# Optimization experiments

Measured on AMD Instinct MI355X. Metric: run time of the kernel, lower is better.

## Reference

```python
import jax, jax.numpy as jnp
import numpy as np

EPS = 1e-8

def div_small(a, b):
    b_safe = b * (b > EPS) + (b <= EPS) * EPS
    return a / b_safe

def cos_full(q1h, q2h, w):
    # q1h [b,s1,h], q2h [b,s1_or_1,h], w [P,h] -> [b,s1,P]
    a = q1h[:, :, None, :] * w          # [b,s1,P,h]
    c = q2h[:, :, None, :] * w          # [b,s1|1,P,h]
    num = jnp.sum(a * c, axis=-1)
    den = jnp.maximum(jnp.linalg.norm(a, axis=-1) * jnp.linalg.norm(c, axis=-1), EPS)
    return num / den

def cos_maxpool(q1h, q2h, w):
    # q1h [b,s1,h], q2h [b,s2,h], w [P,h] -> max over s2 of cosine -> [b,s1,P]
    a = q1h[:, :, None, :] * w          # [b,s1,P,h]
    c = q2h[:, :, None, :] * w          # [b,s2,P,h]
    num = jnp.einsum('biph,bjph->bijp', a, c)            # [b,s1,s2,P]
    na = jnp.linalg.norm(a, axis=-1)                     # [b,s1,P]
    nc = jnp.linalg.norm(c, axis=-1)                     # [b,s2,P]
    den = jnp.maximum(na[:, :, None, :] * nc[:, None, :, :], EPS)
    return jnp.max(num / den, axis=2)

def attention(q1, q2):
    # cosine-similarity matrix [b,s1,s2]
    n1 = jnp.linalg.norm(q1, axis=2, keepdims=True)      # [b,s1,1]
    n2 = jnp.linalg.norm(q2, axis=2, keepdims=True)      # [b,s2,1]
    num = jnp.einsum('bih,bjh->bij', q1, q2)
    return div_small(num, n1 * jnp.swapaxes(n2, 1, 2))

def setup_inputs() -> dict:
    key = jax.random.key(0)
    k1, k2, kw = jax.random.split(key, 3)
    q1_batch = jax.random.normal(k1, (16, 128, 512), dtype=jnp.float32)
    q2_batch = jax.random.normal(k2, (16, 128, 512), dtype=jnp.float32)
    W = jax.random.normal(kw, (8, 16, 256), dtype=jnp.float32)
    return {"q1_batch": q1_batch, "q2_batch": q2_batch, "W": W}

def reference(q1_batch, q2_batch, W):
    h = q1_batch.shape[-1] // 2
    q1_fw, q1_bw = q1_batch[..., :h], q1_batch[..., h:]
    q2_fw, q2_bw = q2_batch[..., :h], q2_batch[..., h:]

    # 1) full matching against last (fw) / first (bw) q2 state
    full_fw = cos_full(q1_fw, q2_fw[:, -1:, :], W[0])
    full_bw = cos_full(q1_bw, q2_bw[:, :1, :], W[1])

    # 2) max-pool matching over all q2 positions
    max_fw = cos_maxpool(q1_fw, q2_fw, W[2])
    max_bw = cos_maxpool(q1_bw, q2_bw, W[3])

    # 3) attentive matching
    att_fw = attention(q1_fw, q2_fw)                     # [b,s1,s2]
    att_bw = attention(q1_bw, q2_bw)
    at_q2_fw = att_fw[..., None] * q2_fw[:, None, :, :]  # [b,s1,s2,h]
    at_q2_bw = att_bw[..., None] * q2_bw[:, None, :, :]
    mean_fw = div_small(at_q2_fw.sum(axis=2), att_fw.sum(axis=2, keepdims=True))
    # NOTE: denominator intentionally uses att_fw (bug preserved from source)
    mean_bw = div_small(at_q2_bw.sum(axis=2), att_fw.sum(axis=2, keepdims=True))
    attn_fw = cos_full(q1_fw, mean_fw, W[4])
    attn_bw = cos_full(q1_bw, mean_bw, W[5])

    # 4) max-attentive matching
    max_at_fw = at_q2_fw.max(axis=2)                     # [b,s1,h]
    max_at_bw = at_q2_bw.max(axis=2)
    maxattn_fw = cos_full(q1_fw, max_at_fw, W[6])
    maxattn_bw = cos_full(q1_bw, max_at_bw, W[7])

    return jnp.concatenate(
        [full_fw, full_bw, max_fw, max_bw, attn_fw, attn_bw, maxattn_fw, maxattn_bw],
        axis=-1)
```

## Files before the change

kernel.cpp:

```cpp
#include <hip/hip_runtime.h>
#include <hip/hip_bf16.h>

#define B 16
#define L 128
#define H 256
#define H2 512
#define P 16
#define EPSF 1e-8f
#define LDSTR 72

typedef __attribute__((ext_vector_type(8))) short short8;
typedef __attribute__((ext_vector_type(4))) short short4v;
typedef __attribute__((ext_vector_type(4))) float f32x4;

__device__ __forceinline__ short f2bf(float x) {
    unsigned u = __builtin_bit_cast(unsigned, x);
    u += 0x7fffu + ((u >> 16) & 1u);
    return (short)(u >> 16);
}
__device__ __forceinline__ float bf2f(short s) {
    unsigned u = ((unsigned)(unsigned short)s) << 16;
    return __builtin_bit_cast(float, u);
}
__device__ __forceinline__ short8 pack8(float4 x, float4 y) {
    short8 s;
    s[0] = f2bf(x.x); s[1] = f2bf(x.y); s[2] = f2bf(x.z); s[3] = f2bf(x.w);
    s[4] = f2bf(y.x); s[5] = f2bf(y.y); s[6] = f2bf(y.z); s[7] = f2bf(y.w);
    return s;
}
__device__ __forceinline__ float dot4(float4 v) {
    return v.x * v.x + v.y * v.y + v.z * v.z + v.w * v.w;
}
__device__ __forceinline__ float4 mul4(float4 a, float4 b) {
    return make_float4(a.x * b.x, a.y * b.y, a.z * b.z, a.w * b.w);
}

__global__ void __launch_bounds__(64) k_att_v3(
        const float* __restrict__ q1, const float* __restrict__ q2,
        float* __restrict__ att_fw, float* __restrict__ att_bw,
        float* __restrict__ attsum) {
    int bx = blockIdx.x;
    int b = bx >> 1, dir = bx & 1;
    int m0 = blockIdx.y * 16, n0 = blockIdx.z * 16;
    int l = threadIdx.x, q = l >> 4, coll = l & 15;
    size_t bL = (size_t)b * L;

    const float* arow = q1 + (bL + m0 + coll) * H2 + dir * H;
    const float* brow = q2 + (bL + n0 + coll) * H2 + dir * H;

    f32x4 acc = (f32x4){0.f, 0.f, 0.f, 0.f};
    float na = 0.f, nc = 0.f;
#pragma unroll
    for (int ks = 0; ks < 8; ks++) {
        int koff = ks * 32 + q * 8;
        float4 a0 = *(const float4*)(arow + koff);
        float4 a1 = *(const float4*)(arow + koff + 4);
        float4 b0 = *(const float4*)(brow + koff);
        float4 b1 = *(const float4*)(brow + koff + 4);
        na += dot4(a0) + dot4(a1);
        nc += dot4(b0) + dot4(b1);
        short8 af = pack8(a0, a1);
        short8 bf = pack8(b0, b1);
        acc = __builtin_amdgcn_mfma_f32_16x16x32_bf16(af, bf, acc, 0, 0, 0);
    }
    na += __shfl_xor(na, 16); na += __shfl_xor(na, 32);
    nc += __shfl_xor(nc, 16); nc += __shfl_xor(nc, 32);
    float na_s = sqrtf(na), nc_s = sqrtf(nc);

    float* attout = dir ? att_bw : att_fw;
    float rsum[4];
#pragma unroll
    for (int r = 0; r < 4; r++) {
        float nar = __shfl(na_s, (l & 48) + q * 4 + r);
        float den = nar * nc_s;
        den = den > EPSF ? den : EPSF;
        float a = acc[r] / den;
        attout[(bL + m0 + q * 4 + r) * L + n0 + coll] = a;
        rsum[r] = a;
    }
    if (dir == 0) {
#pragma unroll
        for (int off = 1; off < 16; off <<= 1)
#pragma unroll
            for (int r = 0; r < 4; r++)
                rsum[r] += __shfl_xor(rsum[r], off, 16);
        if (coll == 0)
#pragma unroll
            for (int r = 0; r < 4; r++)
                atomicAdd(&attsum[bL + m0 + q * 4 + r], rsum[r]);
    }
}

__global__ void __launch_bounds__(256) k_meanmax_v3(
        const float* __restrict__ q2,
        const float* __restrict__ att_fw, const float* __restrict__ att_bw,
        const float* __restrict__ attsum,
        float* __restrict__ mean_fw, float* __restrict__ mean_bw,
        float* __restrict__ maxat_fw, float* __restrict__ maxat_bw) {
    int bd = blockIdx.x;
    int b = bd >> 1, dir = bd & 1;
    int i0 = blockIdx.y * 4;
    int t = threadIdx.x;
    int wave = t >> 6, l = t & 63;
    size_t bL = (size_t)b * L;

    __shared__ float at[4][L];
    __shared__ float Ss[4];
    __shared__ f32x4 red[4][64][4];

    const float* att = dir ? att_bw : att_fw;
    for (int v = t; v < 4 * L; v += 256)
        at[v >> 7][v & 127] = att[(bL + i0 + (v >> 7)) * L + (v & 127)];
    if (t < 4) {
        float s = attsum[bL + i0 + t];
        Ss[t] = s > EPSF ? s : EPSF;
    }
    __syncthreads();

    f32x4 sum[4], mx[4];
#pragma unroll
    for (int r = 0; r < 4; r++) {
        sum[r] = (f32x4){0.f, 0.f, 0.f, 0.f};
        mx[r] = (f32x4){-INFINITY, -INFINITY, -INFINITY, -INFINITY};
    }
    const float* q2b = q2 + bL * H2 + dir * H;
    for (int jj = 0; jj < 32; jj++) {
        int j = wave * 32 + jj;
        float4 c = *(const float4*)(q2b + (size_t)j * H2 + l * 4);
#pragma unroll
        for (int r = 0; r < 4; r++) {
            float w = at[r][j];
            f32x4 v = { w * c.x, w * c.y, w * c.z, w * c.w };
            sum[r] += v;
            mx[r][0] = fmaxf(mx[r][0], v[0]);
            mx[r][1] = fmaxf(mx[r][1], v[1]);
            mx[r][2] = fmaxf(mx[r][2], v[2]);
            mx[r][3] = fmaxf(mx[r][3], v[3]);
        }
    }
    float* meanout = dir ? mean_bw : mean_fw;
    float* maxout = dir ? maxat_bw : maxat_fw;
    for (int rr = 0; rr < 2; rr++) {
        __syncthreads();
        red[wave][l][0] = sum[rr * 2];
        red[wave][l][1] = mx[rr * 2];
        red[wave][l][2] = sum[rr * 2 + 1];
        red[wave][l][3] = mx[rr * 2 + 1];
        __syncthreads();
        if (t < 128) {
            int r2 = t >> 6;
            int lane = t & 63;
            f32x4 s = red[0][lane][r2 * 2];
            f32x4 m = red[0][lane][r2 * 2 + 1];
            for (int w = 1; w < 4; w++) {
                s += red[w][lane][r2 * 2];
                f32x4 m2 = red[w][lane][r2 * 2 + 1];
                m[0] = fmaxf(m[0], m2[0]);
                m[1] = fmaxf(m[1], m2[1]);
                m[2] = fmaxf(m[2], m2[2]);
                m[3] = fmaxf(m[3], m2[3]);
            }
            int row = i0 + rr * 2 + r2;
            float inv = 1.f / Ss[rr * 2 + r2];
            size_t o = (bL + row) * H + lane * 4;
            *(f32x4*)(meanout + o) = s * inv;
            *(f32x4*)(maxout + o) = m;
        }
    }
}

__global__ void __launch_bounds__(256) k_cosfull_v3(
        const float* __restrict__ q1, const float* __restrict__ q2,
        const float* __restrict__ mean_fw, const float* __restrict__ mean_bw,
        const float* __restrict__ maxat_fw, const float* __restrict__ maxat_bw,
        const float* __restrict__ W, float* __restrict__ out) {
    int bg = blockIdx.x;
    int b = bg >> 4;
    int i0 = (bg & 15) * 8;
    int piece = blockIdx.y;
    int t = threadIdx.x;
    int p = t >> 4, l = t & 15;
    size_t bL = (size_t)b * L;

    int widx, colb, dir, cstride;
    const float* cptr;
    switch (piece) {
        case 0: widx = 0; colb = 0;   dir = 0; cptr = q2 + (bL + L - 1) * H2;  cstride = 0; break;
        case 1: widx = 1; colb = 16;  dir = 1; cptr = q2 + bL * H2 + H;        cstride = 0; break;
        case 2: widx = 4; colb = 64;  dir = 0; cptr = mean_fw + bL * H;        cstride = H; break;
        case 3: widx = 5; colb = 80;  dir = 1; cptr = mean_bw + bL * H;        cstride = H; break;
        case 4: widx = 6; colb = 96;  dir = 0; cptr = maxat_fw + bL * H;       cstride = H; break;
        default: widx = 7; colb = 112; dir = 1; cptr = maxat_bw + bL * H;      cstride = H; break;
    }
    const float* wrow = W + ((size_t)widx * P + p) * H;
    float wsq[16];
#pragma unroll
    for (int k = 0; k < 16; k++) {
        float wv = wrow[l + 16 * k];
        wsq[k] = wv * wv;
    }
    for (int ii = 0; ii < 8; ii++) {
        int i = i0 + ii;
        const float* r1 = q1 + (bL + i) * H2 + dir * H;
        const float* crow = cptr + (size_t)i * cstride;
        float num = 0, na = 0, nc = 0;
#pragma unroll
        for (int k = 0; k < 16; k++) {
            int h = l + 16 * k;
            float a = r1[h];
            float c = crow[h];
            num += a * c * wsq[k];
            na  += a * a * wsq[k];
            nc  += c * c * wsq[k];
        }
        for (int off = 8; off; off >>= 1) {
            num += __shfl_down(num, off, 16);
            na  += __shfl_down(na,  off, 16);
            nc  += __shfl_down(nc,  off, 16);
        }
        if (l == 0) {
            float den = sqrtf(na) * sqrtf(nc);
            den = den > EPSF ? den : EPSF;
            out[(bL + i) * 128 + colb + p] = num / den;
        }
    }
}

__global__ void __launch_bounds__(256) k_maxpool_v2(
        const float* __restrict__ q1, const float* __restrict__ q2,
        const float* __restrict__ W, float* __restrict__ out) {
    int bd = blockIdx.x;
    int b = bd >> 1, dir = bd & 1;
    int p = blockIdx.y;
    int t = threadIdx.x;
    int wave = t >> 6, l = t & 63;
    int q = l >> 4, coll = l & 15;
    int m0 = blockIdx.z * 64 + wave * 16;
    size_t bL = (size_t)b * L;

    __shared__ short Bs[128 * LDSTR];
    __shared__ float wf[H];
    __shared__ float ncs[128];

    if (t < 64)
        *(float4*)(wf + t * 4) =
            *(const float4*)(W + ((size_t)(2 + dir) * P + p) * H + t * 4);
    __syncthreads();

    f32x4 acc[8];
#pragma unroll
    for (int nt = 0; nt < 8; nt++) acc[nt] = (f32x4){0.f, 0.f, 0.f, 0.f};
    float ncp = 0.f, nap = 0.f;

    int brow = t >> 1, bc0 = (t & 1) * 32;
    const float* q1b = q1 + bL * H2 + dir * H;
    const float* q2b = q2 + bL * H2 + dir * H;
    const float* arow = q1b + (size_t)(m0 + coll) * H2;
    const float* brp = q2b + (size_t)brow * H2;

    for (int kt = 0; kt < 4; kt++) {
        int k0 = kt * 64;
#pragma unroll
        for (int cc = 0; cc < 8; cc++) {
            float4 v = *(const float4*)(brp + k0 + bc0 + cc * 4);
            float4 wv4 = *(const float4*)(wf + k0 + bc0 + cc * 4);
            float4 x = mul4(v, wv4);
            short4v s = { f2bf(x.x), f2bf(x.y), f2bf(x.z), f2bf(x.w) };
            *(short4v*)(Bs + brow * LDSTR + bc0 + cc * 4) = s;
            float f0 = bf2f(s[0]), f1 = bf2f(s[1]), f2v = bf2f(s[2]), f3 = bf2f(s[3]);
            ncp += f0 * f0 + f1 * f1 + f2v * f2v + f3 * f3;
        }
        __syncthreads();
#pragma unroll
        for (int ks = 0; ks < 2; ks++) {
            int koff = ks * 32 + q * 8;
            float4 a0 = *(const float4*)(arow + k0 + koff);
            float4 a1 = *(const float4*)(arow + k0 + koff + 4);
            float4 w0 = *(const float4*)(wf + k0 + koff);
            float4 w1 = *(const float4*)(wf + k0 + koff + 4);
            float4 e0 = mul4(a0, w0), e1 = mul4(a1, w1);
            short8 af = pack8(e0, e1);
#pragma unroll
            for (int j = 0; j < 8; j++) {
                float f = bf2f(af[j]);
                nap += f * f;
            }
#pragma unroll
            for (int nt = 0; nt < 8; nt++) {
                short8 bf = *(const short8*)(Bs + (nt * 16 + coll) * LDSTR + koff);
                acc[nt] = __builtin_amdgcn_mfma_f32_16x16x32_bf16(af, bf, acc[nt], 0, 0, 0);
            }
        }
        __syncthreads();
    }
    ncp += __shfl_xor(ncp, 1);
    if ((t & 1) == 0) ncs[brow] = sqrtf(ncp);
    nap += __shfl_xor(nap, 16);
    nap += __shfl_xor(nap, 32);
    float na_s = sqrtf(nap);
    __syncthreads();

    float nar[4];
#pragma unroll
    for (int r = 0; r < 4; r++)
        nar[r] = __shfl(na_s, (l & 48) + q * 4 + r);
    float rmax[4] = {-INFINITY, -INFINITY, -INFINITY, -INFINITY};
#pragma unroll
    for (int nt = 0; nt < 8; nt++) {
        float ncv = ncs[nt * 16 + coll];
#pragma unroll
        for (int r = 0; r < 4; r++) {
            float den = fmaxf(nar[r] * ncv, EPSF);
            rmax[r] = fmaxf(rmax[r], acc[nt][r] / den);
        }
    }
#pragma unroll
    for (int off = 1; off < 16; off <<= 1)
#pragma unroll
        for (int r = 0; r < 4; r++)
            rmax[r] = fmaxf(rmax[r], __shfl_xor(rmax[r], off, 16));
    if (coll == 0)
#pragma unroll
        for (int r = 0; r < 4; r++)
            out[(bL + m0 + q * 4 + r) * 128 + 32 + dir * 16 + p] = rmax[r];
}

extern "C" void kernel_launch(void* const* d_in, const int* in_sizes, int n_in,
                              void* d_out, int out_size, void* d_ws, size_t ws_size,
                              hipStream_t stream) {
    const float* q1 = (const float*)d_in[0];
    const float* q2 = (const float*)d_in[1];
    const float* W  = (const float*)d_in[2];
    float* out = (float*)d_out;

    float* ws = (float*)d_ws;
    float* attsum = ws;
    float* att_fw = attsum + B * L;
    float* att_bw = att_fw + (size_t)B * L * L;
    float* mean_fw = att_bw + (size_t)B * L * L;
    float* mean_bw = mean_fw + (size_t)B * L * H;
    float* maxat_fw = mean_bw + (size_t)B * L * H;
    float* maxat_bw = maxat_fw + (size_t)B * L * H;

    hipMemsetAsync(attsum, 0, B * L * sizeof(float), stream);
    k_maxpool_v2<<<dim3(B * 2, P, 2), 256, 0, stream>>>(q1, q2, W, out);
    k_att_v3<<<dim3(B * 2, 8, 8), 64, 0, stream>>>(q1, q2, att_fw, att_bw, attsum);
    k_meanmax_v3<<<dim3(B * 2, 32), 256, 0, stream>>>(q2, att_fw, att_bw, attsum,
                                                      mean_fw, mean_bw, maxat_fw, maxat_bw);
    k_cosfull_v3<<<dim3(B * 16, 6), 256, 0, stream>>>(q1, q2, mean_fw, mean_bw,
                                                      maxat_fw, maxat_bw, W, out);
}
```

Baseline: 132.9 us.

## Stage full weighted q2 tile once per maxpool block, widen meanmax rows, vectorize cosfull

The maxpool kernel now converts the whole 128x256 weighted q2 tile to bf16 in LDS once, then runs both 64-row halves of q1 against it. This halves the grid and removes the per-k-tile barriers and the duplicated B-tile conversion. The meanmax kernel handles 8 rows per block instead of 4, so each q2 load is reused more at the cost of more registers. The cosfull kernel switches to float4 contiguous loads per lane, and the maxpool launch moves to the end of the stream. The larger LDS footprint (about 66KB) and the halved block count may limit occupancy.

```diff
diff --git a/kernel.cpp b/kernel.cpp
--- a/kernel.cpp
+++ b/kernel.cpp
@@ -7,7 +7,7 @@
 #define H2 512
 #define P 16
 #define EPSF 1e-8f
-#define LDSTR 72
+#define LDSTR2 264
 
 typedef __attribute__((ext_vector_type(8))) short short8;
 typedef __attribute__((ext_vector_type(4))) short short4v;
@@ -99,27 +99,27 @@
         float* __restrict__ maxat_fw, float* __restrict__ maxat_bw) {
     int bd = blockIdx.x;
     int b = bd >> 1, dir = bd & 1;
-    int i0 = blockIdx.y * 4;
+    int i0 = blockIdx.y * 8;
     int t = threadIdx.x;
     int wave = t >> 6, l = t & 63;
     size_t bL = (size_t)b * L;
 
-    __shared__ float at[4][L];
-    __shared__ float Ss[4];
+    __shared__ float at[8][L];
+    __shared__ float Ss[8];
     __shared__ f32x4 red[4][64][4];
 
     const float* att = dir ? att_bw : att_fw;
-    for (int v = t; v < 4 * L; v += 256)
+    for (int v = t; v < 8 * L; v += 256)
         at[v >> 7][v & 127] = att[(bL + i0 + (v >> 7)) * L + (v & 127)];
-    if (t < 4) {
+    if (t < 8) {
         float s = attsum[bL + i0 + t];
         Ss[t] = s > EPSF ? s : EPSF;
     }
     __syncthreads();
 
-    f32x4 sum[4], mx[4];
-#pragma unroll
-    for (int r = 0; r < 4; r++) {
+    f32x4 sum[8], mx[8];
+#pragma unroll
+    for (int r = 0; r < 8; r++) {
         sum[r] = (f32x4){0.f, 0.f, 0.f, 0.f};
         mx[r] = (f32x4){-INFINITY, -INFINITY, -INFINITY, -INFINITY};
     }
@@ -128,7 +128,7 @@
         int j = wave * 32 + jj;
         float4 c = *(const float4*)(q2b + (size_t)j * H2 + l * 4);
 #pragma unroll
-        for (int r = 0; r < 4; r++) {
+        for (int r = 0; r < 8; r++) {
             float w = at[r][j];
             f32x4 v = { w * c.x, w * c.y, w * c.z, w * c.w };
             sum[r] += v;
@@ -140,7 +140,7 @@
     }
     float* meanout = dir ? mean_bw : mean_fw;
     float* maxout = dir ? maxat_bw : maxat_fw;
-    for (int rr = 0; rr < 2; rr++) {
+    for (int rr = 0; rr < 4; rr++) {
         __syncthreads();
         red[wave][l][0] = sum[rr * 2];
         red[wave][l][1] = mx[rr * 2];
@@ -169,7 +169,7 @@
     }
 }
 
-__global__ void __launch_bounds__(256) k_cosfull_v3(
+__global__ void __launch_bounds__(256) k_cosfull_v4(
         const float* __restrict__ q1, const float* __restrict__ q2,
         const float* __restrict__ mean_fw, const float* __restrict__ mean_bw,
         const float* __restrict__ maxat_fw, const float* __restrict__ maxat_bw,
@@ -192,26 +192,28 @@
         case 4: widx = 6; colb = 96;  dir = 0; cptr = maxat_fw + bL * H;       cstride = H; break;
         default: widx = 7; colb = 112; dir = 1; cptr = maxat_bw + bL * H;      cstride = H; break;
     }
-    const float* wrow = W + ((size_t)widx * P + p) * H;
-    float wsq[16];
-#pragma unroll
-    for (int k = 0; k < 16; k++) {
-        float wv = wrow[l + 16 * k];
-        wsq[k] = wv * wv;
+    const float* wrow = W + ((size_t)widx * P + p) * H + l * 16;
+    float4 wq[4];
+#pragma unroll
+    for (int c = 0; c < 4; c++) {
+        float4 w4 = *(const float4*)(wrow + c * 4);
+        wq[c] = mul4(w4, w4);
     }
     for (int ii = 0; ii < 8; ii++) {
         int i = i0 + ii;
-        const float* r1 = q1 + (bL + i) * H2 + dir * H;
-        const float* crow = cptr + (size_t)i * cstride;
+        const float* r1 = q1 + (bL + i) * H2 + dir * H + l * 16;
+        const float* crow = cptr + (size_t)i * cstride + l * 16;
         float num = 0, na = 0, nc = 0;
 #pragma unroll
-        for (int k = 0; k < 16; k++) {
-            int h = l + 16 * k;
-            float a = r1[h];
-            float c = crow[h];
-            num += a * c * wsq[k];
-            na  += a * a * wsq[k];
-            nc  += c * c * wsq[k];
+        for (int c = 0; c < 4; c++) {
+            float4 a = *(const float4*)(r1 + c * 4);
+            float4 cc = *(const float4*)(crow + c * 4);
+            num += a.x * cc.x * wq[c].x + a.y * cc.y * wq[c].y
+                 + a.z * cc.z * wq[c].z + a.w * cc.w * wq[c].w;
+            na  += a.x * a.x * wq[c].x + a.y * a.y * wq[c].y
+                 + a.z * a.z * wq[c].z + a.w * a.w * wq[c].w;
+            nc  += cc.x * cc.x * wq[c].x + cc.y * cc.y * wq[c].y
+                 + cc.z * cc.z * wq[c].z + cc.w * cc.w * wq[c].w;
         }
         for (int off = 8; off; off >>= 1) {
             num += __shfl_down(num, off, 16);
@@ -226,7 +228,7 @@
     }
 }
 
-__global__ void __launch_bounds__(256) k_maxpool_v2(
+__global__ void __launch_bounds__(256, 2) k_maxpool_v5(
         const float* __restrict__ q1, const float* __restrict__ q2,
         const float* __restrict__ W, float* __restrict__ out) {
     int bd = blockIdx.x;
@@ -235,29 +237,22 @@
     int t = threadIdx.x;
     int wave = t >> 6, l = t & 63;
     int q = l >> 4, coll = l & 15;
-    int m0 = blockIdx.z * 64 + wave * 16;
     size_t bL = (size_t)b * L;
 
-    __shared__ short Bs[128 * LDSTR];
+    __shared__ short Bs[128 * LDSTR2];
     __shared__ float wf[H];
     __shared__ float ncs[128];
 
+    const float* wbase = W + ((size_t)(2 + dir) * P + p) * H;
     if (t < 64)
-        *(float4*)(wf + t * 4) =
-            *(const float4*)(W + ((size_t)(2 + dir) * P + p) * H + t * 4);
+        *(float4*)(wf + t * 4) = *(const float4*)(wbase + t * 4);
     __syncthreads();
 
-    f32x4 acc[8];
-#pragma unroll
-    for (int nt = 0; nt < 8; nt++) acc[nt] = (f32x4){0.f, 0.f, 0.f, 0.f};
-    float ncp = 0.f, nap = 0.f;
-
     int brow = t >> 1, bc0 = (t & 1) * 32;
-    const float* q1b = q1 + bL * H2 + dir * H;
     const float* q2b = q2 + bL * H2 + dir * H;
-    const float* arow = q1b + (size_t)(m0 + coll) * H2;
     const float* brp = q2b + (size_t)brow * H2;
-
+    float ncp = 0.f;
+#pragma unroll
     for (int kt = 0; kt < 4; kt++) {
         int k0 = kt * 64;
 #pragma unroll
@@ -266,20 +261,30 @@
             float4 wv4 = *(const float4*)(wf + k0 + bc0 + cc * 4);
             float4 x = mul4(v, wv4);
             short4v s = { f2bf(x.x), f2bf(x.y), f2bf(x.z), f2bf(x.w) };
-            *(short4v*)(Bs + brow * LDSTR + bc0 + cc * 4) = s;
+            *(short4v*)(Bs + brow * LDSTR2 + k0 + bc0 + cc * 4) = s;
             float f0 = bf2f(s[0]), f1 = bf2f(s[1]), f2v = bf2f(s[2]), f3 = bf2f(s[3]);
             ncp += f0 * f0 + f1 * f1 + f2v * f2v + f3 * f3;
         }
-        __syncthreads();
-#pragma unroll
-        for (int ks = 0; ks < 2; ks++) {
+    }
+    ncp += __shfl_xor(ncp, 1);
+    if ((t & 1) == 0) ncs[brow] = sqrtf(ncp);
+    __syncthreads();
+
+    for (int half = 0; half < 2; half++) {
+        int m0 = half * 64 + wave * 16;
+        const float* arow = q1 + (bL + m0 + coll) * H2 + dir * H;
+        f32x4 acc[8];
+#pragma unroll
+        for (int nt = 0; nt < 8; nt++) acc[nt] = (f32x4){0.f, 0.f, 0.f, 0.f};
+        float nap = 0.f;
+#pragma unroll
+        for (int ks = 0; ks < 8; ks++) {
             int koff = ks * 32 + q * 8;
-            float4 a0 = *(const float4*)(arow + k0 + koff);
-            float4 a1 = *(const float4*)(arow + k0 + koff + 4);
-            float4 w0 = *(const float4*)(wf + k0 + koff);
-            float4 w1 = *(const float4*)(wf + k0 + koff + 4);
-            float4 e0 = mul4(a0, w0), e1 = mul4(a1, w1);
-            short8 af = pack8(e0, e1);
+            float4 a0 = *(const float4*)(arow + koff);
+            float4 a1 = *(const float4*)(arow + koff + 4);
+            float4 w0 = *(const float4*)(wf + koff);
+            float4 w1 = *(const float4*)(wf + koff + 4);
+            short8 af = pack8(mul4(a0, w0), mul4(a1, w1));
 #pragma unroll
             for (int j = 0; j < 8; j++) {
                 float f = bf2f(af[j]);
@@ -287,42 +292,38 @@
             }
 #pragma unroll
             for (int nt = 0; nt < 8; nt++) {
-                short8 bf = *(const short8*)(Bs + (nt * 16 + coll) * LDSTR + koff);
+                short8 bf = *(const short8*)(Bs + (nt * 16 + coll) * LDSTR2 + koff);
                 acc[nt] = __builtin_amdgcn_mfma_f32_16x16x32_bf16(af, bf, acc[nt], 0, 0, 0);
             }
         }
-        __syncthreads();
-    }
-    ncp += __shfl_xor(ncp, 1);
-    if ((t & 1) == 0) ncs[brow] = sqrtf(ncp);
-    nap += __shfl_xor(nap, 16);
-    nap += __shfl_xor(nap, 32);
-    float na_s = sqrtf(nap);
-    __syncthreads();
-
-    float nar[4];
-#pragma unroll
-    for (int r = 0; r < 4; r++)
-        nar[r] = __shfl(na_s, (l & 48) + q * 4 + r);
-    float rmax[4] = {-INFINITY, -INFINITY, -INFINITY, -INFINITY};
-#pragma unroll
-    for (int nt = 0; nt < 8; nt++) {
-        float ncv = ncs[nt * 16 + coll];
-#pragma unroll
-        for (int r = 0; r < 4; r++) {
-            float den = fmaxf(nar[r] * ncv, EPSF);
-            rmax[r] = fmaxf(rmax[r], acc[nt][r] / den);
-        }
-    }
-#pragma unroll
-    for (int off = 1; off < 16; off <<= 1)
+        nap += __shfl_xor(nap, 16);
+        nap += __shfl_xor(nap, 32);
+        float na_s = sqrtf(nap);
+
+        float nar[4];
 #pragma unroll
         for (int r = 0; r < 4; r++)
-            rmax[r] = fmaxf(rmax[r], __shfl_xor(rmax[r], off, 16));
-    if (coll == 0)
-#pragma unroll
-        for (int r = 0; r < 4; r++)
-            out[(bL + m0 + q * 4 + r) * 128 + 32 + dir * 16 + p] = rmax[r];
+            nar[r] = __shfl(na_s, (l & 48) + q * 4 + r);
+        float rmax[4] = {-INFINITY, -INFINITY, -INFINITY, -INFINITY};
+#pragma unroll
+        for (int nt = 0; nt < 8; nt++) {
+            float ncv = ncs[nt * 16 + coll];
+#pragma unroll
+            for (int r = 0; r < 4; r++) {
+                float den = fmaxf(nar[r] * ncv, EPSF);
+                rmax[r] = fmaxf(rmax[r], acc[nt][r] / den);
+            }
+        }
+#pragma unroll
+        for (int off = 1; off < 16; off <<= 1)
+#pragma unroll
+            for (int r = 0; r < 4; r++)
+                rmax[r] = fmaxf(rmax[r], __shfl_xor(rmax[r], off, 16));
+        if (coll == 0)
+#pragma unroll
+            for (int r = 0; r < 4; r++)
+                out[(bL + m0 + q * 4 + r) * 128 + 32 + dir * 16 + p] = rmax[r];
+    }
 }
 
 extern "C" void kernel_launch(void* const* d_in, const int* in_sizes, int n_in,
@@ -335,18 +336,18 @@
 
     float* ws = (float*)d_ws;
     float* attsum = ws;
-    float* att_fw = attsum + B * L;
+    float* att_fw = attsum + 2048;
     float* att_bw = att_fw + (size_t)B * L * L;
     float* mean_fw = att_bw + (size_t)B * L * L;
     float* mean_bw = mean_fw + (size_t)B * L * H;
     float* maxat_fw = mean_bw + (size_t)B * L * H;
     float* maxat_bw = maxat_fw + (size_t)B * L * H;
 
-    hipMemsetAsync(attsum, 0, B * L * sizeof(float), stream);
-    k_maxpool_v2<<<dim3(B * 2, P, 2), 256, 0, stream>>>(q1, q2, W, out);
+    hipMemsetAsync(attsum, 0, 2048 * sizeof(float), stream);
     k_att_v3<<<dim3(B * 2, 8, 8), 64, 0, stream>>>(q1, q2, att_fw, att_bw, attsum);
-    k_meanmax_v3<<<dim3(B * 2, 32), 256, 0, stream>>>(q2, att_fw, att_bw, attsum,
+    k_meanmax_v3<<<dim3(B * 2, 16), 256, 0, stream>>>(q2, att_fw, att_bw, attsum,
                                                       mean_fw, mean_bw, maxat_fw, maxat_bw);
-    k_cosfull_v3<<<dim3(B * 16, 6), 256, 0, stream>>>(q1, q2, mean_fw, mean_bw,
+    k_cosfull_v4<<<dim3(B * 16, 6), 256, 0, stream>>>(q1, q2, mean_fw, mean_bw,
                                                       maxat_fw, maxat_bw, W, out);
-}
+    k_maxpool_v5<<<dim3(B * 2, P), 256, 0, stream>>>(q1, q2, W, out);
+}
```

New measurement: 170.2 us. 1.28x slower.

## Fuse mean/max attentive reduction with cosine full-matching into one kernel

Applied to the files above, without the earlier changes.

Merges the mean/max attentive aggregation kernel and the full-matching cosine kernel into a single kernel. Per-row mean and max vectors now stay in shared memory instead of a global workspace round trip, and one launch is removed. Each block now handles 8 query rows instead of 4, which halves the block count and raises register use for the sum/max accumulators. It also computes three cosine outputs (full, mean, max-attentive) per thread with vectorized loads, and reorders launches so the attention kernel runs before max-pool.

```diff
diff --git a/kernel.cpp b/kernel.cpp
--- a/kernel.cpp
+++ b/kernel.cpp
@@ -91,35 +91,135 @@
     }
 }
 
-__global__ void __launch_bounds__(256) k_meanmax_v3(
-        const float* __restrict__ q2,
+__global__ void __launch_bounds__(256) k_maxpool_v2(
+        const float* __restrict__ q1, const float* __restrict__ q2,
+        const float* __restrict__ W, float* __restrict__ out) {
+    int bd = blockIdx.x;
+    int b = bd >> 1, dir = bd & 1;
+    int p = blockIdx.y;
+    int t = threadIdx.x;
+    int wave = t >> 6, l = t & 63;
+    int q = l >> 4, coll = l & 15;
+    int m0 = blockIdx.z * 64 + wave * 16;
+    size_t bL = (size_t)b * L;
+
+    __shared__ short Bs[128 * LDSTR];
+    __shared__ float wf[H];
+    __shared__ float ncs[128];
+
+    if (t < 64)
+        *(float4*)(wf + t * 4) =
+            *(const float4*)(W + ((size_t)(2 + dir) * P + p) * H + t * 4);
+    __syncthreads();
+
+    f32x4 acc[8];
+#pragma unroll
+    for (int nt = 0; nt < 8; nt++) acc[nt] = (f32x4){0.f, 0.f, 0.f, 0.f};
+    float ncp = 0.f, nap = 0.f;
+
+    int brow = t >> 1, bc0 = (t & 1) * 32;
+    const float* q1b = q1 + bL * H2 + dir * H;
+    const float* q2b = q2 + bL * H2 + dir * H;
+    const float* arow = q1b + (size_t)(m0 + coll) * H2;
+    const float* brp = q2b + (size_t)brow * H2;
+
+    for (int kt = 0; kt < 4; kt++) {
+        int k0 = kt * 64;
+#pragma unroll
+        for (int cc = 0; cc < 8; cc++) {
+            float4 v = *(const float4*)(brp + k0 + bc0 + cc * 4);
+            float4 wv4 = *(const float4*)(wf + k0 + bc0 + cc * 4);
+            float4 x = mul4(v, wv4);
+            short4v s = { f2bf(x.x), f2bf(x.y), f2bf(x.z), f2bf(x.w) };
+            *(short4v*)(Bs + brow * LDSTR + bc0 + cc * 4) = s;
+            float f0 = bf2f(s[0]), f1 = bf2f(s[1]), f2v = bf2f(s[2]), f3 = bf2f(s[3]);
+            ncp += f0 * f0 + f1 * f1 + f2v * f2v + f3 * f3;
+        }
+        __syncthreads();
+#pragma unroll
+        for (int ks = 0; ks < 2; ks++) {
+            int koff = ks * 32 + q * 8;
+            float4 a0 = *(const float4*)(arow + k0 + koff);
+            float4 a1 = *(const float4*)(arow + k0 + koff + 4);
+            float4 w0 = *(const float4*)(wf + k0 + koff);
+            float4 w1 = *(const float4*)(wf + k0 + koff + 4);
+            float4 e0 = mul4(a0, w0), e1 = mul4(a1, w1);
+            short8 af = pack8(e0, e1);
+#pragma unroll
+            for (int j = 0; j < 8; j++) {
+                float f = bf2f(af[j]);
+                nap += f * f;
+            }
+#pragma unroll
+            for (int nt = 0; nt < 8; nt++) {
+                short8 bf = *(const short8*)(Bs + (nt * 16 + coll) * LDSTR + koff);
+                acc[nt] = __builtin_amdgcn_mfma_f32_16x16x32_bf16(af, bf, acc[nt], 0, 0, 0);
+            }
+        }
+        __syncthreads();
+    }
+    ncp += __shfl_xor(ncp, 1);
+    if ((t & 1) == 0) ncs[brow] = sqrtf(ncp);
+    nap += __shfl_xor(nap, 16);
+    nap += __shfl_xor(nap, 32);
+    float na_s = sqrtf(nap);
+    __syncthreads();
+
+    float nar[4];
+#pragma unroll
+    for (int r = 0; r < 4; r++)
+        nar[r] = __shfl(na_s, (l & 48) + q * 4 + r);
+    float rmax[4] = {-INFINITY, -INFINITY, -INFINITY, -INFINITY};
+#pragma unroll
+    for (int nt = 0; nt < 8; nt++) {
+        float ncv = ncs[nt * 16 + coll];
+#pragma unroll
+        for (int r = 0; r < 4; r++) {
+            float den = fmaxf(nar[r] * ncv, EPSF);
+            rmax[r] = fmaxf(rmax[r], acc[nt][r] / den);
+        }
+    }
+#pragma unroll
+    for (int off = 1; off < 16; off <<= 1)
+#pragma unroll
+        for (int r = 0; r < 4; r++)
+            rmax[r] = fmaxf(rmax[r], __shfl_xor(rmax[r], off, 16));
+    if (coll == 0)
+#pragma unroll
+        for (int r = 0; r < 4; r++)
+            out[(bL + m0 + q * 4 + r) * 128 + 32 + dir * 16 + p] = rmax[r];
+}
+
+__global__ void __launch_bounds__(256) k_mmcos(
+        const float* __restrict__ q1, const float* __restrict__ q2,
         const float* __restrict__ att_fw, const float* __restrict__ att_bw,
         const float* __restrict__ attsum,
-        float* __restrict__ mean_fw, float* __restrict__ mean_bw,
-        float* __restrict__ maxat_fw, float* __restrict__ maxat_bw) {
+        const float* __restrict__ W, float* __restrict__ out) {
     int bd = blockIdx.x;
     int b = bd >> 1, dir = bd & 1;
-    int i0 = blockIdx.y * 4;
+    int i0 = blockIdx.y * 8;
     int t = threadIdx.x;
     int wave = t >> 6, l = t & 63;
     size_t bL = (size_t)b * L;
 
-    __shared__ float at[4][L];
-    __shared__ float Ss[4];
+    __shared__ float at[8][L];
+    __shared__ float Ss[8];
     __shared__ f32x4 red[4][64][4];
+    __shared__ float meanL[8][H];
+    __shared__ float maxL[8][H];
 
     const float* att = dir ? att_bw : att_fw;
-    for (int v = t; v < 4 * L; v += 256)
+    for (int v = t; v < 8 * L; v += 256)
         at[v >> 7][v & 127] = att[(bL + i0 + (v >> 7)) * L + (v & 127)];
-    if (t < 4) {
+    if (t < 8) {
         float s = attsum[bL + i0 + t];
         Ss[t] = s > EPSF ? s : EPSF;
     }
     __syncthreads();
 
-    f32x4 sum[4], mx[4];
-#pragma unroll
-    for (int r = 0; r < 4; r++) {
+    f32x4 sum[8], mx[8];
+#pragma unroll
+    for (int r = 0; r < 8; r++) {
         sum[r] = (f32x4){0.f, 0.f, 0.f, 0.f};
         mx[r] = (f32x4){-INFINITY, -INFINITY, -INFINITY, -INFINITY};
     }
@@ -128,7 +228,7 @@
         int j = wave * 32 + jj;
         float4 c = *(const float4*)(q2b + (size_t)j * H2 + l * 4);
 #pragma unroll
-        for (int r = 0; r < 4; r++) {
+        for (int r = 0; r < 8; r++) {
             float w = at[r][j];
             f32x4 v = { w * c.x, w * c.y, w * c.z, w * c.w };
             sum[r] += v;
@@ -138,9 +238,7 @@
             mx[r][3] = fmaxf(mx[r][3], v[3]);
         }
     }
-    float* meanout = dir ? mean_bw : mean_fw;
-    float* maxout = dir ? maxat_bw : maxat_fw;
-    for (int rr = 0; rr < 2; rr++) {
+    for (int rr = 0; rr < 4; rr++) {
         __syncthreads();
         red[wave][l][0] = sum[rr * 2];
         red[wave][l][1] = mx[rr * 2];
@@ -160,169 +258,85 @@
                 m[2] = fmaxf(m[2], m2[2]);
                 m[3] = fmaxf(m[3], m2[3]);
             }
-            int row = i0 + rr * 2 + r2;
-            float inv = 1.f / Ss[rr * 2 + r2];
-            size_t o = (bL + row) * H + lane * 4;
-            *(f32x4*)(meanout + o) = s * inv;
-            *(f32x4*)(maxout + o) = m;
-        }
-    }
-}
-
-__global__ void __launch_bounds__(256) k_cosfull_v3(
-        const float* __restrict__ q1, const float* __restrict__ q2,
-        const float* __restrict__ mean_fw, const float* __restrict__ mean_bw,
-        const float* __restrict__ maxat_fw, const float* __restrict__ maxat_bw,
-        const float* __restrict__ W, float* __restrict__ out) {
-    int bg = blockIdx.x;
-    int b = bg >> 4;
-    int i0 = (bg & 15) * 8;
-    int piece = blockIdx.y;
-    int t = threadIdx.x;
-    int p = t >> 4, l = t & 15;
-    size_t bL = (size_t)b * L;
-
-    int widx, colb, dir, cstride;
-    const float* cptr;
-    switch (piece) {
-        case 0: widx = 0; colb = 0;   dir = 0; cptr = q2 + (bL + L - 1) * H2;  cstride = 0; break;
-        case 1: widx = 1; colb = 16;  dir = 1; cptr = q2 + bL * H2 + H;        cstride = 0; break;
-        case 2: widx = 4; colb = 64;  dir = 0; cptr = mean_fw + bL * H;        cstride = H; break;
-        case 3: widx = 5; colb = 80;  dir = 1; cptr = mean_bw + bL * H;        cstride = H; break;
-        case 4: widx = 6; colb = 96;  dir = 0; cptr = maxat_fw + bL * H;       cstride = H; break;
-        default: widx = 7; colb = 112; dir = 1; cptr = maxat_bw + bL * H;      cstride = H; break;
-    }
-    const float* wrow = W + ((size_t)widx * P + p) * H;
-    float wsq[16];
-#pragma unroll
-    for (int k = 0; k < 16; k++) {
-        float wv = wrow[l + 16 * k];
-        wsq[k] = wv * wv;
-    }
+            int r = rr * 2 + r2;
+            float inv = 1.f / Ss[r];
+            *(f32x4*)(&meanL[r][lane * 4]) = s * inv;
+            *(f32x4*)(&maxL[r][lane * 4]) = m;
+        }
+    }
+    __syncthreads();
+
+    int p = t >> 4, li = t & 15;
+    float4 wqA[4], wqB[4], wqC[4];
+#pragma unroll
+    for (int c = 0; c < 4; c++) {
+        float4 wA = *(const float4*)(W + ((size_t)dir * P + p) * H + li * 16 + c * 4);
+        float4 wB = *(const float4*)(W + ((size_t)(4 + dir) * P + p) * H + li * 16 + c * 4);
+        float4 wC = *(const float4*)(W + ((size_t)(6 + dir) * P + p) * H + li * 16 + c * 4);
+        wqA[c] = mul4(wA, wA);
+        wqB[c] = mul4(wB, wB);
+        wqC[c] = mul4(wC, wC);
+    }
+    const float* q2end = q2 + (bL + (dir ? 0 : (L - 1))) * H2 + dir * H + li * 16;
+    float4 ce[4];
+#pragma unroll
+    for (int c = 0; c < 4; c++) ce[c] = *(const float4*)(q2end + c * 4);
+
     for (int ii = 0; ii < 8; ii++) {
         int i = i0 + ii;
-        const float* r1 = q1 + (bL + i) * H2 + dir * H;
-        const float* crow = cptr + (size_t)i * cstride;
-        float num = 0, na = 0, nc = 0;
-#pragma unroll
-        for (int k = 0; k < 16; k++) {
-            int h = l + 16 * k;
-            float a = r1[h];
-            float c = crow[h];
-            num += a * c * wsq[k];
-            na  += a * a * wsq[k];
-            nc  += c * c * wsq[k];
+        const float* r1 = q1 + (bL + i) * H2 + dir * H + li * 16;
+        float4 a[4];
+#pragma unroll
+        for (int c = 0; c < 4; c++) a[c] = *(const float4*)(r1 + c * 4);
+
+        float numA = 0, naA = 0, ncA = 0;
+        float numB = 0, naB = 0, ncB = 0;
+        float numC = 0, naC = 0, ncC = 0;
+#pragma unroll
+        for (int c = 0; c < 4; c++) {
+            float4 cm = *(const float4*)(&meanL[ii][li * 16 + c * 4]);
+            float4 cx = *(const float4*)(&maxL[ii][li * 16 + c * 4]);
+            float4 av = a[c], cv = ce[c];
+            numA += av.x * cv.x * wqA[c].x + av.y * cv.y * wqA[c].y
+                  + av.z * cv.z * wqA[c].z + av.w * cv.w * wqA[c].w;
+            naA  += av.x * av.x * wqA[c].x + av.y * av.y * wqA[c].y
+                  + av.z * av.z * wqA[c].z + av.w * av.w * wqA[c].w;
+            ncA  += cv.x * cv.x * wqA[c].x + cv.y * cv.y * wqA[c].y
+                  + cv.z * cv.z * wqA[c].z + cv.w * cv.w * wqA[c].w;
+            numB += av.x * cm.x * wqB[c].x + av.y * cm.y * wqB[c].y
+                  + av.z * cm.z * wqB[c].z + av.w * cm.w * wqB[c].w;
+            naB  += av.x * av.x * wqB[c].x + av.y * av.y * wqB[c].y
+                  + av.z * av.z * wqB[c].z + av.w * av.w * wqB[c].w;
+            ncB  += cm.x * cm.x * wqB[c].x + cm.y * cm.y * wqB[c].y
+                  + cm.z * cm.z * wqB[c].z + cm.w * cm.w * wqB[c].w;
+            numC += av.x * cx.x * wqC[c].x + av.y * cx.y * wqC[c].y
+                  + av.z * cx.z * wqC[c].z + av.w * cx.w * wqC[c].w;
+            naC  += av.x * av.x * wqC[c].x + av.y * av.y * wqC[c].y
+                  + av.z * av.z * wqC[c].z + av.w * av.w * wqC[c].w;
+            ncC  += cx.x * cx.x * wqC[c].x + cx.y * cx.y * wqC[c].y
+                  + cx.z * cx.z * wqC[c].z + cx.w * cx.w * wqC[c].w;
         }
         for (int off = 8; off; off >>= 1) {
-            num += __shfl_down(num, off, 16);
-            na  += __shfl_down(na,  off, 16);
-            nc  += __shfl_down(nc,  off, 16);
-        }
-        if (l == 0) {
-            float den = sqrtf(na) * sqrtf(nc);
-            den = den > EPSF ? den : EPSF;
-            out[(bL + i) * 128 + colb + p] = num / den;
-        }
-    }
-}
-
-__global__ void __launch_bounds__(256) k_maxpool_v2(
-        const float* __restrict__ q1, const float* __restrict__ q2,
-        const float* __restrict__ W, float* __restrict__ out) {
-    int bd = blockIdx.x;
-    int b = bd >> 1, dir = bd & 1;
-    int p = blockIdx.y;
-    int t = threadIdx.x;
-    int wave = t >> 6, l = t & 63;
-    int q = l >> 4, coll = l & 15;
-    int m0 = blockIdx.z * 64 + wave * 16;
-    size_t bL = (size_t)b * L;
-
-    __shared__ short Bs[128 * LDSTR];
-    __shared__ float wf[H];
-    __shared__ float ncs[128];
-
-    if (t < 64)
-        *(float4*)(wf + t * 4) =
-            *(const float4*)(W + ((size_t)(2 + dir) * P + p) * H + t * 4);
-    __syncthreads();
-
-    f32x4 acc[8];
-#pragma unroll
-    for (int nt = 0; nt < 8; nt++) acc[nt] = (f32x4){0.f, 0.f, 0.f, 0.f};
-    float ncp = 0.f, nap = 0.f;
-
-    int brow = t >> 1, bc0 = (t & 1) * 32;
-    const float* q1b = q1 + bL * H2 + dir * H;
-    const float* q2b = q2 + bL * H2 + dir * H;
-    const float* arow = q1b + (size_t)(m0 + coll) * H2;
-    const float* brp = q2b + (size_t)brow * H2;
-
-    for (int kt = 0; kt < 4; kt++) {
-        int k0 = kt * 64;
-#pragma unroll
-        for (int cc = 0; cc < 8; cc++) {
-            float4 v = *(const float4*)(brp + k0 + bc0 + cc * 4);
-            float4 wv4 = *(const float4*)(wf + k0 + bc0 + cc * 4);
-            float4 x = mul4(v, wv4);
-            short4v s = { f2bf(x.x), f2bf(x.y), f2bf(x.z), f2bf(x.w) };
-            *(short4v*)(Bs + brow * LDSTR + bc0 + cc * 4) = s;
-            float f0 = bf2f(s[0]), f1 = bf2f(s[1]), f2v = bf2f(s[2]), f3 = bf2f(s[3]);
-            ncp += f0 * f0 + f1 * f1 + f2v * f2v + f3 * f3;
-        }
-        __syncthreads();
-#pragma unroll
-        for (int ks = 0; ks < 2; ks++) {
-            int koff = ks * 32 + q * 8;
-            float4 a0 = *(const float4*)(arow + k0 + koff);
-            float4 a1 = *(const float4*)(arow + k0 + koff + 4);
-            float4 w0 = *(const float4*)(wf + k0 + koff);
-            float4 w1 = *(const float4*)(wf + k0 + koff + 4);
-            float4 e0 = mul4(a0, w0), e1 = mul4(a1, w1);
-            short8 af = pack8(e0, e1);
-#pragma unroll
-            for (int j = 0; j < 8; j++) {
-                float f = bf2f(af[j]);
-                nap += f * f;
-            }
-#pragma unroll
-            for (int nt = 0; nt < 8; nt++) {
-                short8 bf = *(const short8*)(Bs + (nt * 16 + coll) * LDSTR + koff);
-                acc[nt] = __builtin_amdgcn_mfma_f32_16x16x32_bf16(af, bf, acc[nt], 0, 0, 0);
-            }
-        }
-        __syncthreads();
-    }
-    ncp += __shfl_xor(ncp, 1);
-    if ((t & 1) == 0) ncs[brow] = sqrtf(ncp);
-    nap += __shfl_xor(nap, 16);
-    nap += __shfl_xor(nap, 32);
-    float na_s = sqrtf(nap);
-    __syncthreads();
-
-    float nar[4];
-#pragma unroll
-    for (int r = 0; r < 4; r++)
-        nar[r] = __shfl(na_s, (l & 48) + q * 4 + r);
-    float rmax[4] = {-INFINITY, -INFINITY, -INFINITY, -INFINITY};
-#pragma unroll
-    for (int nt = 0; nt < 8; nt++) {
-        float ncv = ncs[nt * 16 + coll];
-#pragma unroll
-        for (int r = 0; r < 4; r++) {
-            float den = fmaxf(nar[r] * ncv, EPSF);
-            rmax[r] = fmaxf(rmax[r], acc[nt][r] / den);
-        }
-    }
-#pragma unroll
-    for (int off = 1; off < 16; off <<= 1)
-#pragma unroll
-        for (int r = 0; r < 4; r++)
-            rmax[r] = fmaxf(rmax[r], __shfl_xor(rmax[r], off, 16));
-    if (coll == 0)
-#pragma unroll
-        for (int r = 0; r < 4; r++)
-            out[(bL + m0 + q * 4 + r) * 128 + 32 + dir * 16 + p] = rmax[r];
+            numA += __shfl_down(numA, off, 16);
+            naA  += __shfl_down(naA,  off, 16);
+            ncA  += __shfl_down(ncA,  off, 16);
+            numB += __shfl_down(numB, off, 16);
+            naB  += __shfl_down(naB,  off, 16);
+            ncB  += __shfl_down(ncB,  off, 16);
+            numC += __shfl_down(numC, off, 16);
+            naC  += __shfl_down(naC,  off, 16);
+            ncC  += __shfl_down(ncC,  off, 16);
+        }
+        if (li == 0) {
+            float dA = sqrtf(naA) * sqrtf(ncA); dA = dA > EPSF ? dA : EPSF;
+            float dB = sqrtf(naB) * sqrtf(ncB); dB = dB > EPSF ? dB : EPSF;
+            float dC = sqrtf(naC) * sqrtf(ncC); dC = dC > EPSF ? dC : EPSF;
+            float* orow = out + (bL + i) * 128;
+            orow[16 * dir + p] = numA / dA;
+            orow[64 + 16 * dir + p] = numB / dB;
+            orow[96 + 16 * dir + p] = numC / dC;
+        }
+    }
 }
 
 extern "C" void kernel_launch(void* const* d_in, const int* in_sizes, int n_in,
@@ -335,18 +349,12 @@
 
     float* ws = (float*)d_ws;
     float* attsum = ws;
-    float* att_fw = attsum + B * L;
+    float* att_fw = attsum + 2048;
     float* att_bw = att_fw + (size_t)B * L * L;
-    float* mean_fw = att_bw + (size_t)B * L * L;
-    float* mean_bw = mean_fw + (size_t)B * L * H;
-    float* maxat_fw = mean_bw + (size_t)B * L * H;
-    float* maxat_bw = maxat_fw + (size_t)B * L * H;
-
-    hipMemsetAsync(attsum, 0, B * L * sizeof(float), stream);
+
+    hipMemsetAsync(attsum, 0, 2048 * sizeof(float), stream);
+    k_att_v3<<<dim3(B * 2, 8, 8), 64, 0, stream>>>(q1, q2, att_fw, att_bw, attsum);
     k_maxpool_v2<<<dim3(B * 2, P, 2), 256, 0, stream>>>(q1, q2, W, out);
-    k_att_v3<<<dim3(B * 2, 8, 8), 64, 0, stream>>>(q1, q2, att_fw, att_bw, attsum);
-    k_meanmax_v3<<<dim3(B * 2, 32), 256, 0, stream>>>(q2, att_fw, att_bw, attsum,
-                                                      mean_fw, mean_bw, maxat_fw, maxat_bw);
-    k_cosfull_v3<<<dim3(B * 16, 6), 256, 0, stream>>>(q1, q2, mean_fw, mean_bw,
-                                                      maxat_fw, maxat_bw, W, out);
-}
+    k_mmcos<<<dim3(B * 2, 16), 256, 0, stream>>>(q1, q2, att_fw, att_bw, attsum,
+                                                 W, out);
+}
```

Measured after the change: 135.7 us. 2.1% more time.
